# Kernel tuning notes

Hardware: AMD Instinct MI355X
Metric: run time of the kernel (lower is better)

## Reference

```python
import jax, jax.numpy as jnp
import numpy as np

N_TOKENS, D_MODEL, D_FF, TOP_K, N_EXPERTS = 8192, 1024, 4096, 2, 8
CAPACITY_FACTOR = 2.0  # static capacity; with uniform routing overflow prob is ~0 (>40 sigma)


def setup_inputs() -> dict:
    key = jax.random.key(0)
    k_x, k_idx, k_w, k1, k2, k3 = jax.random.split(key, 6)
    std_in = (1.0 / 3.0) ** 0.5 / (D_MODEL ** 0.5)   # fan_in = d_model for w1, w2
    std_out = (1.0 / 3.0) ** 0.5 / (D_FF ** 0.5)      # fan_in = d_ff for w3
    x = jax.random.normal(k_x, (N_TOKENS, D_MODEL), jnp.float32)
    expert_indices = jax.random.randint(k_idx, (N_TOKENS, TOP_K), 0, N_EXPERTS)
    expert_weights = jax.random.uniform(k_w, (N_TOKENS, TOP_K), jnp.float32)
    w1 = jax.random.truncated_normal(k1, -2.0, 2.0, (N_EXPERTS, D_MODEL, D_FF), jnp.float32) * std_in
    w2 = jax.random.truncated_normal(k2, -2.0, 2.0, (N_EXPERTS, D_MODEL, D_FF), jnp.float32) * std_in
    w3 = jax.random.truncated_normal(k3, -2.0, 2.0, (N_EXPERTS, D_FF, D_MODEL), jnp.float32) * std_out
    return {"x": x, "expert_indices": expert_indices, "expert_weights": expert_weights,
            "w1": w1, "w2": w2, "w3": w3}


def reference(x, expert_indices, expert_weights, w1, w2, w3):
    n_tokens, d_model = x.shape
    n_experts = w1.shape[0]
    top_k = expert_indices.shape[1]
    total = n_tokens * top_k
    cap = int(CAPACITY_FACTOR * total / n_experts)  # static per-expert capacity (stands in for dynamic max_count)

    flat_experts = expert_indices.reshape(-1)                      # [total]
    flat_weights = expert_weights.reshape(-1)                      # [total]
    token_indices = jnp.repeat(jnp.arange(n_tokens), top_k)        # [total], matches expand+reshape

    order = jnp.argsort(flat_experts, stable=True)
    sorted_tok = token_indices[order]
    sorted_eid = flat_experts[order]
    sorted_wts = flat_weights[order]

    counts = jnp.bincount(flat_experts, length=n_experts)
    seg_starts = jnp.concatenate([jnp.zeros((1,), counts.dtype), jnp.cumsum(counts)[:-1]])
    positions = jnp.arange(total) - seg_starts[sorted_eid]         # slot within expert segment
    valid = positions < cap
    pos_c = jnp.minimum(positions, cap)                             # overflow goes to dump row `cap`

    # dispatch: [n_experts, cap+1, d_model] (last row is dump slot)
    padded = jnp.zeros((n_experts, cap + 1, d_model), x.dtype).at[sorted_eid, pos_c].set(x[sorted_tok])

    # per-expert SwiGLU FFN (grouped GEMMs)
    gate = jax.nn.silu(jnp.einsum('ecd,edf->ecf', padded, w1))
    value = jnp.einsum('ecd,edf->ecf', padded, w2)
    expert_out = jnp.einsum('ecf,efd->ecd', gate * value, w3)       # [n_experts, cap+1, d_model]

    gathered = expert_out[sorted_eid, pos_c]                        # [total, d_model]
    gathered = gathered * jnp.where(valid, sorted_wts, 0.0)[:, None]

    return jnp.zeros((n_tokens, d_model), x.dtype).at[sorted_tok].add(gathered)
```

## Files before the change

kernel.cpp:

```cpp
#include <hip/hip_runtime.h>
#include <stdint.h>

#define N_TOKENS  8192
#define D_MODEL   1024
#define D_FF      4096
#define TOP_K     2
#define N_EXPERTS 8
#define TOTAL_SLOTS (N_TOKENS * TOP_K)
#define CAP       4096
#define ROWS_PAD  (TOTAL_SLOTS + 128)

typedef unsigned short u16;
typedef __attribute__((ext_vector_type(4))) float f32x4;
typedef __attribute__((ext_vector_type(8))) short bf16x8;

__device__ __forceinline__ float bf2f(u16 u) {
  union { unsigned int i; float f; } v; v.i = ((unsigned int)u) << 16; return v.f;
}
__device__ __forceinline__ u16 f2bf(float f) {
  union { float f; unsigned int i; } v; v.f = f;
  unsigned int u = v.i;
  return (u16)((u + 0x7FFFu + ((u >> 16) & 1u)) >> 16);
}

__device__ __forceinline__ void gld_lds16(const void* g, void* l) {
  __builtin_amdgcn_global_load_lds(
      (const __attribute__((address_space(1))) unsigned int*)g,
      (__attribute__((address_space(3))) unsigned int*)l,
      16, 0, 0);
}

__global__ __launch_bounds__(256) void k_route(const int* __restrict__ eidx,
                                               int* __restrict__ info,
                                               int* __restrict__ row_of_slot,
                                               int* __restrict__ tok_of_row) {
  __shared__ int s_total[N_EXPERTS];
  __shared__ int s_start[N_EXPERTS];
  __shared__ int s_base[N_EXPERTS];
  __shared__ int s_wcnt[4][N_EXPERTS];
  const int t = threadIdx.x;
  const int lane = t & 63;
  const int w = t >> 6;

  if (t < N_EXPERTS) { s_total[t] = 0; s_base[t] = 0; }
  __syncthreads();

  for (int c = 0; c < TOTAL_SLOTS / 256; ++c) {
    int e = eidx[c * 256 + t];
    atomicAdd(&s_total[e], 1);
  }
  __syncthreads();

  if (t == 0) {
    int off = 0;
    for (int e = 0; e < N_EXPERTS; ++e) {
      int placed = s_total[e] < CAP ? s_total[e] : CAP;
      s_start[e] = off;
      info[e] = placed;
      info[N_EXPERTS + e] = off;
      off += placed;
    }
    info[2 * N_EXPERTS] = off;
  }
  __syncthreads();

  for (int c = 0; c < TOTAL_SLOTS / 256; ++c) {
    int s = c * 256 + t;
    int e = eidx[s];
    unsigned long long mymask = 0;
    for (int ee = 0; ee < N_EXPERTS; ++ee) {
      unsigned long long m = __ballot(e == ee);
      if (ee == e) mymask = m;
      if (lane == 0) s_wcnt[w][ee] = __popcll(m);
    }
    int rank_in_wave = __popcll(mymask & ((1ULL << lane) - 1ULL));
    __syncthreads();
    int prior = 0;
    for (int ww = 0; ww < w; ++ww) prior += s_wcnt[ww][e];
    int pos = s_base[e] + prior + rank_in_wave;
    int row = (pos < CAP) ? (s_start[e] + pos) : -1;
    row_of_slot[s] = row;
    if (row >= 0) tok_of_row[row] = s >> 1;
    __syncthreads();
    if (t < N_EXPERTS) {
      int tot = 0;
      for (int ww = 0; ww < 4; ++ww) tot += s_wcnt[ww][t];
      s_base[t] += tot;
    }
    __syncthreads();
  }
}

__global__ __launch_bounds__(256) void k_transpose(const float* __restrict__ in,
                                                   u16* __restrict__ out,
                                                   int R, int C) {
  __shared__ float tile[64][65];
  const int e = blockIdx.z;
  in  += (size_t)e * R * C;
  out += (size_t)e * R * C;
  const int c0 = blockIdx.x * 64;
  const int r0 = blockIdx.y * 64;
  const int tx = threadIdx.x & 15, ty = threadIdx.x >> 4;

  #pragma unroll
  for (int rr = 0; rr < 4; ++rr) {
    int r = ty + rr * 16;
    float4 v = *(const float4*)&in[(size_t)(r0 + r) * C + c0 + tx * 4];
    tile[r][tx * 4 + 0] = v.x; tile[r][tx * 4 + 1] = v.y;
    tile[r][tx * 4 + 2] = v.z; tile[r][tx * 4 + 3] = v.w;
  }
  __syncthreads();
  #pragma unroll
  for (int rr = 0; rr < 4; ++rr) {
    int oc = ty + rr * 16;
    ushort4 o;
    o.x = f2bf(tile[tx * 4 + 0][oc]);
    o.y = f2bf(tile[tx * 4 + 1][oc]);
    o.z = f2bf(tile[tx * 4 + 2][oc]);
    o.w = f2bf(tile[tx * 4 + 3][oc]);
    *(ushort4*)&out[(size_t)(c0 + oc) * R + r0 + tx * 4] = o;
  }
}

__global__ __launch_bounds__(256) void k_dispatch(const float* __restrict__ x,
                                                  const int* __restrict__ tok_of_row,
                                                  const int* __restrict__ info,
                                                  u16* __restrict__ Xd) {
  const int r = blockIdx.x;
  const int t = threadIdx.x;
  const int total = info[2 * N_EXPERTS];
  if (r >= total) {
    ushort4 z = {0, 0, 0, 0};
    *(ushort4*)&Xd[(size_t)r * D_MODEL + t * 4] = z;
    return;
  }
  int tok = tok_of_row[r];
  float4 v = *(const float4*)&x[(size_t)tok * D_MODEL + t * 4];
  ushort4 o;
  o.x = f2bf(v.x); o.y = f2bf(v.y); o.z = f2bf(v.z); o.w = f2bf(v.w);
  *(ushort4*)&Xd[(size_t)r * D_MODEL + t * 4] = o;
}

__global__ __launch_bounds__(256, 2) void k_ffn1(const u16* __restrict__ Xd,
                                                 const u16* __restrict__ W1t,
                                                 const u16* __restrict__ W2t,
                                                 u16* __restrict__ H,
                                                 const int* __restrict__ info) {
  const int e = blockIdx.z;
  const int count = info[e];
  const int row0 = blockIdx.y * 128;
  if (row0 >= count) return;
  const int start = info[N_EXPERTS + e];
  const int col0 = blockIdx.x * 128;

  __shared__ u16 lsA[128 * 64];
  __shared__ u16 lsB1[128 * 64];
  __shared__ u16 lsB2[128 * 64];

  const int t = threadIdx.x, lane = t & 63, wid = t >> 6;
  const int wr = wid >> 1, wc = wid & 1;

  const u16* gA  = Xd  + (size_t)(start + row0) * D_MODEL;
  const u16* gB1 = W1t + (size_t)e * D_FF * D_MODEL + (size_t)col0 * D_MODEL;
  const u16* gB2 = W2t + (size_t)e * D_FF * D_MODEL + (size_t)col0 * D_MODEL;

  f32x4 accG[4][4] = {};
  f32x4 accV[4][4] = {};

  const int srow = wid * 8 + (lane >> 3);
  const int skk  = (lane & 7) * 8;

  for (int k0 = 0; k0 < D_MODEL; k0 += 64) {
    __syncthreads();
    #pragma unroll
    for (int i = 0; i < 4; ++i) {
      int r = i * 32 + srow;
      int lbase = (i * 32 + wid * 8) * 64;
      gld_lds16(gA  + (size_t)r * D_MODEL + k0 + skk, &lsA[lbase]);
      gld_lds16(gB1 + (size_t)r * D_MODEL + k0 + skk, &lsB1[lbase]);
      gld_lds16(gB2 + (size_t)r * D_MODEL + k0 + skk, &lsB2[lbase]);
    }
    __syncthreads();
    #pragma unroll
    for (int kk = 0; kk < 2; ++kk) {
      bf16x8 a[4];
      #pragma unroll
      for (int m = 0; m < 4; ++m)
        a[m] = *(const bf16x8*)&lsA[(wr * 64 + m * 16 + (lane & 15)) * 64 + kk * 32 + (lane >> 4) * 8];
      #pragma unroll
      for (int n = 0; n < 4; ++n) {
        bf16x8 b1 = *(const bf16x8*)&lsB1[(wc * 64 + n * 16 + (lane & 15)) * 64 + kk * 32 + (lane >> 4) * 8];
        bf16x8 b2 = *(const bf16x8*)&lsB2[(wc * 64 + n * 16 + (lane & 15)) * 64 + kk * 32 + (lane >> 4) * 8];
        #pragma unroll
        for (int m = 0; m < 4; ++m) {
          accG[m][n] = __builtin_amdgcn_mfma_f32_16x16x32_bf16(a[m], b1, accG[m][n], 0, 0, 0);
          accV[m][n] = __builtin_amdgcn_mfma_f32_16x16x32_bf16(a[m], b2, accV[m][n], 0, 0, 0);
        }
      }
    }
  }

  const int rmax = count - row0;
  const size_t hbase = (size_t)(start + row0);
  #pragma unroll
  for (int m = 0; m < 4; ++m) {
    #pragma unroll
    for (int j = 0; j < 4; ++j) {
      int rit = wr * 64 + m * 16 + (lane >> 4) * 4 + j;
      if (rit < rmax) {
        #pragma unroll
        for (int n = 0; n < 4; ++n) {
          float g = accG[m][n][j];
          float v = accV[m][n][j];
          float h = g * v / (1.0f + __expf(-g));
          H[(hbase + rit) * D_FF + col0 + wc * 64 + n * 16 + (lane & 15)] = f2bf(h);
        }
      }
    }
  }
}

__global__ __launch_bounds__(256) void k_ffn2(const u16* __restrict__ Hbuf,
                                              const u16* __restrict__ W3t,
                                              u16* __restrict__ Y,
                                              const int* __restrict__ info) {
  const int e = blockIdx.z;
  const int count = info[e];
  const int row0 = blockIdx.y * 128;
  if (row0 >= count) return;
  const int start = info[N_EXPERTS + e];
  const int col0 = blockIdx.x * 128;

  __shared__ u16 lsA[128 * 64];
  __shared__ u16 lsB[128 * 64];

  const int t = threadIdx.x, lane = t & 63, wid = t >> 6;
  const int wr = wid >> 1, wc = wid & 1;

  const u16* gA = Hbuf + (size_t)(start + row0) * D_FF;
  const u16* gB = W3t + (size_t)e * D_MODEL * D_FF + (size_t)col0 * D_FF;

  f32x4 acc[4][4] = {};

  const int srow = wid * 8 + (lane >> 3);
  const int skk  = (lane & 7) * 8;

  for (int k0 = 0; k0 < D_FF; k0 += 64) {
    __syncthreads();
    #pragma unroll
    for (int i = 0; i < 4; ++i) {
      int r = i * 32 + srow;
      int lbase = (i * 32 + wid * 8) * 64;
      gld_lds16(gA + (size_t)r * D_FF + k0 + skk, &lsA[lbase]);
      gld_lds16(gB + (size_t)r * D_FF + k0 + skk, &lsB[lbase]);
    }
    __syncthreads();
    #pragma unroll
    for (int kk = 0; kk < 2; ++kk) {
      bf16x8 a[4];
      #pragma unroll
      for (int m = 0; m < 4; ++m)
        a[m] = *(const bf16x8*)&lsA[(wr * 64 + m * 16 + (lane & 15)) * 64 + kk * 32 + (lane >> 4) * 8];
      #pragma unroll
      for (int n = 0; n < 4; ++n) {
        bf16x8 b = *(const bf16x8*)&lsB[(wc * 64 + n * 16 + (lane & 15)) * 64 + kk * 32 + (lane >> 4) * 8];
        #pragma unroll
        for (int m = 0; m < 4; ++m)
          acc[m][n] = __builtin_amdgcn_mfma_f32_16x16x32_bf16(a[m], b, acc[m][n], 0, 0, 0);
      }
    }
  }

  const int rmax = count - row0;
  const size_t ybase = (size_t)(start + row0);
  #pragma unroll
  for (int m = 0; m < 4; ++m) {
    #pragma unroll
    for (int j = 0; j < 4; ++j) {
      int rit = wr * 64 + m * 16 + (lane >> 4) * 4 + j;
      if (rit < rmax) {
        #pragma unroll
        for (int n = 0; n < 4; ++n)
          Y[(ybase + rit) * D_MODEL + col0 + wc * 64 + n * 16 + (lane & 15)] = f2bf(acc[m][n][j]);
      }
    }
  }
}

__global__ __launch_bounds__(256) void k_combine(const u16* __restrict__ Y,
                                                 const int* __restrict__ row_of_slot,
                                                 const float* __restrict__ ew,
                                                 float* __restrict__ out) {
  const int tok = blockIdx.x;
  const int c = threadIdx.x * 4;
  const int r0 = row_of_slot[tok * 2 + 0];
  const int r1 = row_of_slot[tok * 2 + 1];
  const float w0 = ew[tok * 2 + 0];
  const float w1 = ew[tok * 2 + 1];
  float a0 = 0.f, a1 = 0.f, a2 = 0.f, a3 = 0.f;
  if (r0 >= 0) {
    ushort4 y = *(const ushort4*)&Y[(size_t)r0 * D_MODEL + c];
    a0 = w0 * bf2f(y.x); a1 = w0 * bf2f(y.y); a2 = w0 * bf2f(y.z); a3 = w0 * bf2f(y.w);
  }
  if (r1 >= 0) {
    ushort4 y = *(const ushort4*)&Y[(size_t)r1 * D_MODEL + c];
    a0 += w1 * bf2f(y.x); a1 += w1 * bf2f(y.y); a2 += w1 * bf2f(y.z); a3 += w1 * bf2f(y.w);
  }
  float4 o; o.x = a0; o.y = a1; o.z = a2; o.w = a3;
  *(float4*)&out[(size_t)tok * D_MODEL + c] = o;
}

extern "C" void kernel_launch(void* const* d_in, const int* in_sizes, int n_in,
                              void* d_out, int out_size, void* d_ws, size_t ws_size,
                              hipStream_t stream) {
  const float* x  = (const float*)d_in[0];
  const int*   ei = (const int*)d_in[1];
  const float* ew = (const float*)d_in[2];
  const float* w1 = (const float*)d_in[3];
  const float* w2 = (const float*)d_in[4];
  const float* w3 = (const float*)d_in[5];
  float* out = (float*)d_out;

  char* ws = (char*)d_ws;
  size_t off = 0;
  auto alloc = [&](size_t b) { char* p = ws + off; off += (b + 255) & ~(size_t)255; return p; };
  int* info        = (int*)alloc(256);
  int* row_of_slot = (int*)alloc(sizeof(int) * TOTAL_SLOTS);
  int* tok_of_row  = (int*)alloc(sizeof(int) * ROWS_PAD);
  u16* Xd  = (u16*)alloc((size_t)2 * ROWS_PAD * D_MODEL);
  u16* W1t = (u16*)alloc((size_t)2 * N_EXPERTS * D_FF * D_MODEL);
  u16* W2t = (u16*)alloc((size_t)2 * N_EXPERTS * D_FF * D_MODEL);
  u16* W3t = (u16*)alloc((size_t)2 * N_EXPERTS * D_FF * D_MODEL);
  u16* H   = (u16*)alloc((size_t)2 * ROWS_PAD * D_FF);
  u16* Y   = (u16*)alloc((size_t)2 * ROWS_PAD * D_MODEL);

  k_route<<<1, 256, 0, stream>>>(ei, info, row_of_slot, tok_of_row);
  k_transpose<<<dim3(D_FF / 64, D_MODEL / 64, N_EXPERTS), 256, 0, stream>>>(w1, W1t, D_MODEL, D_FF);
  k_transpose<<<dim3(D_FF / 64, D_MODEL / 64, N_EXPERTS), 256, 0, stream>>>(w2, W2t, D_MODEL, D_FF);
  k_transpose<<<dim3(D_MODEL / 64, D_FF / 64, N_EXPERTS), 256, 0, stream>>>(w3, W3t, D_FF, D_MODEL);
  k_dispatch<<<ROWS_PAD, 256, 0, stream>>>(x, tok_of_row, info, Xd);
  k_ffn1<<<dim3(D_FF / 128, CAP / 128, N_EXPERTS), 256, 0, stream>>>(Xd, W1t, W2t, H, info);
  k_ffn2<<<dim3(D_MODEL / 128, CAP / 128, N_EXPERTS), 256, 0, stream>>>(H, W3t, Y, info);
  k_combine<<<N_TOKENS, 256, 0, stream>>>(Y, row_of_slot, ew, out);
}
```

Measured before the change: 823.7 us.

## Replace FFN GEMMs with 256x256 double-buffered, swizzled 8-wave MFMA kernel

Replaces the two 128x128 expert GEMM kernels with one templated 256x256 tile kernel using 512 threads. It double-buffers LDS with split half-K phases and fine-grained vmcnt waits, XOR-swizzles the LDS layout to avoid bank conflicts, and raises MFMA priority. The gate and value weights are interleaved into a single concatenated B matrix in 32-column groups, so one GEMM produces both for the SwiGLU epilogue. Larger tiles raise arithmetic intensity and the pipeline overlaps loads with compute. In exchange, rows are padded to 256 (more wasted work on partial tiles) and register pressure goes up.

```diff
diff --git a/kernel.cpp b/kernel.cpp
--- a/kernel.cpp
+++ b/kernel.cpp
@@ -8,7 +8,7 @@
 #define N_EXPERTS 8
 #define TOTAL_SLOTS (N_TOKENS * TOP_K)
 #define CAP       4096
-#define ROWS_PAD  (TOTAL_SLOTS + 128)
+#define ROWS_PAD  (TOTAL_SLOTS + 384)
 
 typedef unsigned short u16;
 typedef __attribute__((ext_vector_type(4))) float f32x4;
@@ -91,13 +91,14 @@
   }
 }
 
+template<int MODE, int OSTRIDE>
 __global__ __launch_bounds__(256) void k_transpose(const float* __restrict__ in,
                                                    u16* __restrict__ out,
                                                    int R, int C) {
   __shared__ float tile[64][65];
   const int e = blockIdx.z;
   in  += (size_t)e * R * C;
-  out += (size_t)e * R * C;
+  out += (size_t)e * OSTRIDE;
   const int c0 = blockIdx.x * 64;
   const int r0 = blockIdx.y * 64;
   const int tx = threadIdx.x & 15, ty = threadIdx.x >> 4;
@@ -118,7 +119,10 @@
     o.y = f2bf(tile[tx * 4 + 1][oc]);
     o.z = f2bf(tile[tx * 4 + 2][oc]);
     o.w = f2bf(tile[tx * 4 + 3][oc]);
-    *(ushort4*)&out[(size_t)(c0 + oc) * R + r0 + tx * 4] = o;
+    int c = c0 + oc;
+    size_t orow = (MODE == 0) ? (size_t)c
+                              : (size_t)(c >> 5) * 64 + (MODE == 2 ? 32 : 0) + (c & 31);
+    *(ushort4*)&out[orow * R + r0 + tx * 4] = o;
   }
 }
 
@@ -141,147 +145,122 @@
   *(ushort4*)&Xd[(size_t)r * D_MODEL + t * 4] = o;
 }
 
-__global__ __launch_bounds__(256, 2) void k_ffn1(const u16* __restrict__ Xd,
-                                                 const u16* __restrict__ W1t,
-                                                 const u16* __restrict__ W2t,
-                                                 u16* __restrict__ H,
-                                                 const int* __restrict__ info) {
+template<int K, int NB, bool DUAL>
+__global__ __launch_bounds__(512, 2) void k_gemm8(const u16* __restrict__ A,
+                                                  const u16* __restrict__ B,
+                                                  u16* __restrict__ OUT,
+                                                  const int* __restrict__ info) {
   const int e = blockIdx.z;
   const int count = info[e];
-  const int row0 = blockIdx.y * 128;
+  const int row0 = blockIdx.y * 256;
   if (row0 >= count) return;
   const int start = info[N_EXPERTS + e];
-  const int col0 = blockIdx.x * 128;
-
-  __shared__ u16 lsA[128 * 64];
-  __shared__ u16 lsB1[128 * 64];
-  __shared__ u16 lsB2[128 * 64];
-
-  const int t = threadIdx.x, lane = t & 63, wid = t >> 6;
-  const int wr = wid >> 1, wc = wid & 1;
-
-  const u16* gA  = Xd  + (size_t)(start + row0) * D_MODEL;
-  const u16* gB1 = W1t + (size_t)e * D_FF * D_MODEL + (size_t)col0 * D_MODEL;
-  const u16* gB2 = W2t + (size_t)e * D_FF * D_MODEL + (size_t)col0 * D_MODEL;
-
-  f32x4 accG[4][4] = {};
-  f32x4 accV[4][4] = {};
-
-  const int srow = wid * 8 + (lane >> 3);
-  const int skk  = (lane & 7) * 8;
-
-  for (int k0 = 0; k0 < D_MODEL; k0 += 64) {
-    __syncthreads();
+  const int col0 = blockIdx.x * 256;
+
+  __shared__ u16 lsA[2][2][256 * 32];
+  __shared__ u16 lsB[2][2][256 * 32];
+
+  const int tid = threadIdx.x;
+  const int lane = tid & 63, wid = tid >> 6;
+  const int wm = wid >> 2, wn = wid & 3;
+  const int l15 = lane & 15;
+  const int aslot = (lane >> 4) ^ ((l15 >> 1) & 3);
+
+  const u16* gA = A + (size_t)(start + row0) * K;
+  const u16* gB = B + ((size_t)e * NB + col0) * K;
+
+  f32x4 acc[8][4] = {};
+
+  auto stageA = [&](int kt, int h, int bufi) {
+    const int koff = kt * 64 + h * 32;
     #pragma unroll
-    for (int i = 0; i < 4; ++i) {
-      int r = i * 32 + srow;
-      int lbase = (i * 32 + wid * 8) * 64;
-      gld_lds16(gA  + (size_t)r * D_MODEL + k0 + skk, &lsA[lbase]);
-      gld_lds16(gB1 + (size_t)r * D_MODEL + k0 + skk, &lsB1[lbase]);
-      gld_lds16(gB2 + (size_t)r * D_MODEL + k0 + skk, &lsB2[lbase]);
-    }
-    __syncthreads();
+    for (int j = 0; j < 2; ++j) {
+      const int q = j * 8 + wid;
+      const int r = q * 16 + (lane >> 2);
+      const int c = (lane & 3) ^ ((r >> 1) & 3);
+      gld_lds16(gA + (size_t)r * K + koff + c * 8, (void*)&lsA[bufi][h][q * 512]);
+    }
+  };
+  auto stageB = [&](int kt, int h, int bufi) {
+    const int koff = kt * 64 + h * 32;
     #pragma unroll
-    for (int kk = 0; kk < 2; ++kk) {
-      bf16x8 a[4];
+    for (int j = 0; j < 2; ++j) {
+      const int q = j * 8 + wid;
+      const int r = q * 16 + (lane >> 2);
+      const int c = (lane & 3) ^ ((r >> 1) & 3);
+      gld_lds16(gB + (size_t)r * K + koff + c * 8, (void*)&lsB[bufi][h][q * 512]);
+    }
+  };
+
+#define PHASE(HK, NH, STAGE_STMT)                                              \
+  do {                                                                         \
+    STAGE_STMT;                                                                \
+    asm volatile("s_waitcnt vmcnt(6)" ::: "memory");                           \
+    asm volatile("s_barrier" ::: "memory");                                    \
+    __builtin_amdgcn_sched_barrier(0);                                         \
+    const u16* bApt = &lsA[buf][HK][0];                                        \
+    const u16* bBpt = &lsB[buf][HK][0];                                        \
+    bf16x8 a[8], bb[2];                                                        \
+    _Pragma("unroll")                                                          \
+    for (int m = 0; m < 8; ++m)                                                \
+      a[m] = *(const bf16x8*)&bApt[(wm * 128 + m * 16 + l15) * 32 + aslot * 8];\
+    _Pragma("unroll")                                                          \
+    for (int n = 0; n < 2; ++n)                                                \
+      bb[n] = *(const bf16x8*)&bBpt[(wn * 64 + (NH * 2 + n) * 16 + l15) * 32 + aslot * 8]; \
+    __builtin_amdgcn_s_setprio(1);                                             \
+    _Pragma("unroll")                                                          \
+    for (int m = 0; m < 8; ++m) {                                              \
+      acc[m][NH * 2 + 0] = __builtin_amdgcn_mfma_f32_16x16x32_bf16(a[m], bb[0], acc[m][NH * 2 + 0], 0, 0, 0); \
+      acc[m][NH * 2 + 1] = __builtin_amdgcn_mfma_f32_16x16x32_bf16(a[m], bb[1], acc[m][NH * 2 + 1], 0, 0, 0); \
+    }                                                                          \
+    __builtin_amdgcn_s_setprio(0);                                             \
+  } while (0)
+
+  stageA(0, 0, 0); stageB(0, 0, 0); stageA(0, 1, 0); stageB(0, 1, 0);
+
+  constexpr int NT = K / 64;
+  for (int t = 0; t < NT; ++t) {
+    const int buf = t & 1, nbuf = buf ^ 1;
+    const int tn = (t + 1 < NT) ? (t + 1) : t;
+    PHASE(0, 0, stageA(tn, 0, nbuf));
+    PHASE(0, 1, stageB(tn, 0, nbuf));
+    PHASE(1, 0, stageA(tn, 1, nbuf));
+    PHASE(1, 1, stageB(tn, 1, nbuf));
+  }
+  asm volatile("s_waitcnt vmcnt(0)" ::: "memory");
+#undef PHASE
+
+  const int rmax = count - row0;
+  const size_t obase = (size_t)(start + row0);
+  if (DUAL) {
+    const int ffbase = ((col0 >> 6) + wn) * 32 + l15;
+    #pragma unroll
+    for (int m = 0; m < 8; ++m) {
       #pragma unroll
-      for (int m = 0; m < 4; ++m)
-        a[m] = *(const bf16x8*)&lsA[(wr * 64 + m * 16 + (lane & 15)) * 64 + kk * 32 + (lane >> 4) * 8];
-      #pragma unroll
-      for (int n = 0; n < 4; ++n) {
-        bf16x8 b1 = *(const bf16x8*)&lsB1[(wc * 64 + n * 16 + (lane & 15)) * 64 + kk * 32 + (lane >> 4) * 8];
-        bf16x8 b2 = *(const bf16x8*)&lsB2[(wc * 64 + n * 16 + (lane & 15)) * 64 + kk * 32 + (lane >> 4) * 8];
-        #pragma unroll
-        for (int m = 0; m < 4; ++m) {
-          accG[m][n] = __builtin_amdgcn_mfma_f32_16x16x32_bf16(a[m], b1, accG[m][n], 0, 0, 0);
-          accV[m][n] = __builtin_amdgcn_mfma_f32_16x16x32_bf16(a[m], b2, accV[m][n], 0, 0, 0);
+      for (int j = 0; j < 4; ++j) {
+        int rit = wm * 128 + m * 16 + (lane >> 4) * 4 + j;
+        if (rit < rmax) {
+          #pragma unroll
+          for (int n = 0; n < 2; ++n) {
+            float g = acc[m][n][j];
+            float v = acc[m][n + 2][j];
+            float h = g * v / (1.0f + __expf(-g));
+            OUT[(obase + rit) * D_FF + ffbase + n * 16] = f2bf(h);
+          }
         }
       }
     }
-  }
-
-  const int rmax = count - row0;
-  const size_t hbase = (size_t)(start + row0);
-  #pragma unroll
-  for (int m = 0; m < 4; ++m) {
+  } else {
     #pragma unroll
-    for (int j = 0; j < 4; ++j) {
-      int rit = wr * 64 + m * 16 + (lane >> 4) * 4 + j;
-      if (rit < rmax) {
-        #pragma unroll
-        for (int n = 0; n < 4; ++n) {
-          float g = accG[m][n][j];
-          float v = accV[m][n][j];
-          float h = g * v / (1.0f + __expf(-g));
-          H[(hbase + rit) * D_FF + col0 + wc * 64 + n * 16 + (lane & 15)] = f2bf(h);
+    for (int m = 0; m < 8; ++m) {
+      #pragma unroll
+      for (int j = 0; j < 4; ++j) {
+        int rit = wm * 128 + m * 16 + (lane >> 4) * 4 + j;
+        if (rit < rmax) {
+          #pragma unroll
+          for (int n = 0; n < 4; ++n)
+            OUT[(obase + rit) * D_MODEL + col0 + wn * 64 + n * 16 + l15] = f2bf(acc[m][n][j]);
         }
-      }
-    }
-  }
-}
-
-__global__ __launch_bounds__(256) void k_ffn2(const u16* __restrict__ Hbuf,
-                                              const u16* __restrict__ W3t,
-                                              u16* __restrict__ Y,
-                                              const int* __restrict__ info) {
-  const int e = blockIdx.z;
-  const int count = info[e];
-  const int row0 = blockIdx.y * 128;
-  if (row0 >= count) return;
-  const int start = info[N_EXPERTS + e];
-  const int col0 = blockIdx.x * 128;
-
-  __shared__ u16 lsA[128 * 64];
-  __shared__ u16 lsB[128 * 64];
-
-  const int t = threadIdx.x, lane = t & 63, wid = t >> 6;
-  const int wr = wid >> 1, wc = wid & 1;
-
-  const u16* gA = Hbuf + (size_t)(start + row0) * D_FF;
-  const u16* gB = W3t + (size_t)e * D_MODEL * D_FF + (size_t)col0 * D_FF;
-
-  f32x4 acc[4][4] = {};
-
-  const int srow = wid * 8 + (lane >> 3);
-  const int skk  = (lane & 7) * 8;
-
-  for (int k0 = 0; k0 < D_FF; k0 += 64) {
-    __syncthreads();
-    #pragma unroll
-    for (int i = 0; i < 4; ++i) {
-      int r = i * 32 + srow;
-      int lbase = (i * 32 + wid * 8) * 64;
-      gld_lds16(gA + (size_t)r * D_FF + k0 + skk, &lsA[lbase]);
-      gld_lds16(gB + (size_t)r * D_FF + k0 + skk, &lsB[lbase]);
-    }
-    __syncthreads();
-    #pragma unroll
-    for (int kk = 0; kk < 2; ++kk) {
-      bf16x8 a[4];
-      #pragma unroll
-      for (int m = 0; m < 4; ++m)
-        a[m] = *(const bf16x8*)&lsA[(wr * 64 + m * 16 + (lane & 15)) * 64 + kk * 32 + (lane >> 4) * 8];
-      #pragma unroll
-      for (int n = 0; n < 4; ++n) {
-        bf16x8 b = *(const bf16x8*)&lsB[(wc * 64 + n * 16 + (lane & 15)) * 64 + kk * 32 + (lane >> 4) * 8];
-        #pragma unroll
-        for (int m = 0; m < 4; ++m)
-          acc[m][n] = __builtin_amdgcn_mfma_f32_16x16x32_bf16(a[m], b, acc[m][n], 0, 0, 0);
-      }
-    }
-  }
-
-  const int rmax = count - row0;
-  const size_t ybase = (size_t)(start + row0);
-  #pragma unroll
-  for (int m = 0; m < 4; ++m) {
-    #pragma unroll
-    for (int j = 0; j < 4; ++j) {
-      int rit = wr * 64 + m * 16 + (lane >> 4) * 4 + j;
-      if (rit < rmax) {
-        #pragma unroll
-        for (int n = 0; n < 4; ++n)
-          Y[(ybase + rit) * D_MODEL + col0 + wc * 64 + n * 16 + (lane & 15)] = f2bf(acc[m][n][j]);
       }
     }
   }
@@ -327,19 +306,18 @@
   int* info        = (int*)alloc(256);
   int* row_of_slot = (int*)alloc(sizeof(int) * TOTAL_SLOTS);
   int* tok_of_row  = (int*)alloc(sizeof(int) * ROWS_PAD);
-  u16* Xd  = (u16*)alloc((size_t)2 * ROWS_PAD * D_MODEL);
-  u16* W1t = (u16*)alloc((size_t)2 * N_EXPERTS * D_FF * D_MODEL);
-  u16* W2t = (u16*)alloc((size_t)2 * N_EXPERTS * D_FF * D_MODEL);
-  u16* W3t = (u16*)alloc((size_t)2 * N_EXPERTS * D_FF * D_MODEL);
-  u16* H   = (u16*)alloc((size_t)2 * ROWS_PAD * D_FF);
-  u16* Y   = (u16*)alloc((size_t)2 * ROWS_PAD * D_MODEL);
+  u16* Xd   = (u16*)alloc((size_t)2 * ROWS_PAD * D_MODEL);
+  u16* W12t = (u16*)alloc((size_t)2 * N_EXPERTS * 2 * D_FF * D_MODEL);
+  u16* W3t  = (u16*)alloc((size_t)2 * N_EXPERTS * D_FF * D_MODEL);
+  u16* H    = (u16*)alloc((size_t)2 * ROWS_PAD * D_FF);
+  u16* Y    = (u16*)alloc((size_t)2 * ROWS_PAD * D_MODEL);
 
   k_route<<<1, 256, 0, stream>>>(ei, info, row_of_slot, tok_of_row);
-  k_transpose<<<dim3(D_FF / 64, D_MODEL / 64, N_EXPERTS), 256, 0, stream>>>(w1, W1t, D_MODEL, D_FF);
-  k_transpose<<<dim3(D_FF / 64, D_MODEL / 64, N_EXPERTS), 256, 0, stream>>>(w2, W2t, D_MODEL, D_FF);
-  k_transpose<<<dim3(D_MODEL / 64, D_FF / 64, N_EXPERTS), 256, 0, stream>>>(w3, W3t, D_FF, D_MODEL);
+  k_transpose<1, 2 * D_FF * D_MODEL><<<dim3(D_FF / 64, D_MODEL / 64, N_EXPERTS), 256, 0, stream>>>(w1, W12t, D_MODEL, D_FF);
+  k_transpose<2, 2 * D_FF * D_MODEL><<<dim3(D_FF / 64, D_MODEL / 64, N_EXPERTS), 256, 0, stream>>>(w2, W12t, D_MODEL, D_FF);
+  k_transpose<0, D_FF * D_MODEL><<<dim3(D_MODEL / 64, D_FF / 64, N_EXPERTS), 256, 0, stream>>>(w3, W3t, D_FF, D_MODEL);
   k_dispatch<<<ROWS_PAD, 256, 0, stream>>>(x, tok_of_row, info, Xd);
-  k_ffn1<<<dim3(D_FF / 128, CAP / 128, N_EXPERTS), 256, 0, stream>>>(Xd, W1t, W2t, H, info);
-  k_ffn2<<<dim3(D_MODEL / 128, CAP / 128, N_EXPERTS), 256, 0, stream>>>(H, W3t, Y, info);
+  k_gemm8<D_MODEL, 2 * D_FF, true><<<dim3(2 * D_FF / 256, CAP / 256, N_EXPERTS), 512, 0, stream>>>(Xd, W12t, H, info);
+  k_gemm8<D_FF, D_MODEL, false><<<dim3(D_MODEL / 256, CAP / 256, N_EXPERTS), 512, 0, stream>>>(H, W3t, Y, info);
   k_combine<<<N_TOKENS, 256, 0, stream>>>(Y, row_of_slot, ew, out);
 }
```

After: 864.7 us. 5.0% more time.
